# Kernel tuning notes

Hardware: AMD Instinct MI355X
Metric: run time of the kernel (lower is better)

The kernel has to match this reference:

```python
import jax, jax.numpy as jnp
import numpy as np

NEG_SLOPE = 0.2  # PyG GATConv default leaky_relu slope


def segment_softmax(logits, seg, num_segments):
    # logits: [E, H], seg: [E] destination node ids
    m = jax.ops.segment_max(logits, seg, num_segments=num_segments)
    m = jnp.where(jnp.isfinite(m), m, 0.0)  # empty segments
    e = jnp.exp(logits - m[seg])
    s = jax.ops.segment_sum(e, seg, num_segments=num_segments)
    return e / (s[seg] + 1e-16)


def gat_conv(x, src, dst, W, att_src, att_dst, bias, heads, out_ch, concat, num_nodes):
    # x: [N, F_in], W: [F_in, heads*out_ch], att_*: [heads, out_ch]
    h = (x @ W).reshape(num_nodes, heads, out_ch)            # [N, H, C]
    a_src = jnp.sum(h * att_src, axis=-1)                    # [N, H]
    a_dst = jnp.sum(h * att_dst, axis=-1)                    # [N, H]
    logits = jax.nn.leaky_relu(a_src[src] + a_dst[dst], NEG_SLOPE)  # [E, H]
    alpha = segment_softmax(logits, dst, num_nodes)          # [E, H]
    msg = h[src] * alpha[..., None]                          # [E, H, C]
    out = jax.ops.segment_sum(msg, dst, num_segments=num_nodes)  # [N, H, C]
    out = out.reshape(num_nodes, heads * out_ch) if concat else out.mean(axis=1)
    return out + bias


def setup_inputs() -> dict:
    key = jax.random.key(0)
    ks = jax.random.split(key, 12)
    N, E = 50000, 800000
    F_in, Hd, H, F_out = 256, 128, 2, 64

    def glorot(k, shape):
        fan = shape[0] + shape[-1]
        return jax.random.normal(k, shape, dtype=jnp.float32) * jnp.sqrt(2.0 / fan)

    x = jax.random.normal(ks[0], (N, F_in), dtype=jnp.float32)
    edge_index = jax.random.randint(ks[1], (2, E), 0, N, dtype=jnp.int32)
    return {
        "x": x,
        "edge_index": edge_index,
        "W1": glorot(ks[2], (F_in, H * Hd)),
        "att_src1": glorot(ks[3], (H, Hd)),
        "att_dst1": glorot(ks[4], (H, Hd)),
        "b1": jnp.zeros((H * Hd,), dtype=jnp.float32),
        "W2": glorot(ks[5], (H * Hd, F_out)),
        "att_src2": glorot(ks[6], (1, F_out)),
        "att_dst2": glorot(ks[7], (1, F_out)),
        "b2": jnp.zeros((F_out,), dtype=jnp.float32),
    }


def reference(x, edge_index, W1, att_src1, att_dst1, b1, W2, att_src2, att_dst2, b2):
    N = x.shape[0]
    # PyG GATConv default: add self loops
    ar = jnp.arange(N, dtype=edge_index.dtype)
    src = jnp.concatenate([edge_index[0], ar])
    dst = jnp.concatenate([edge_index[1], ar])
    # dropout layers are identity in eval mode
    h = gat_conv(x, src, dst, W1, att_src1, att_dst1, b1,
                 heads=2, out_ch=128, concat=True, num_nodes=N)
    h = jax.nn.elu(h)
    out = gat_conv(h, src, dst, W2, att_src2, att_dst2, b2,
                   heads=1, out_ch=64, concat=False, num_nodes=N)
    return jax.nn.log_softmax(out, axis=1)
```

## Files before the change

kernel.cpp:

```cpp
#include <hip/hip_runtime.h>
#include <hip/hip_bf16.h>

typedef unsigned short u16;
typedef short bf8_t __attribute__((ext_vector_type(8)));
typedef float f32x4 __attribute__((ext_vector_type(4)));

__device__ inline u16 f2bf(float f) {
  unsigned u = __float_as_uint(f);
  u += 0x7FFFu + ((u >> 16) & 1u);
  return (u16)(u >> 16);
}
__device__ inline float bf2f(u16 h) { return __uint_as_float(((unsigned)h) << 16); }
__device__ inline float bflo(unsigned u) { return __uint_as_float(u << 16); }
__device__ inline float bfhi(unsigned u) { return __uint_as_float(u & 0xffff0000u); }

__global__ void prep_kernel(const int* __restrict__ ei, int E, int N, int N8,
                            int* __restrict__ counts,
                            const float* __restrict__ W1, const float* __restrict__ W2,
                            u16* __restrict__ W1T, u16* __restrict__ W2T, int teamBlocks) {
  if ((int)blockIdx.x < teamBlocks) {
    const int team = blockIdx.x & 7;
    const int tslot = blockIdx.x >> 3;
    const int TB = teamBlocks >> 3;
    const int lo = team * N8, hi = min(N, lo + N8);
    const int Et = E + N;
    for (int e = tslot * 256 + (int)threadIdx.x; e < Et; e += TB * 256) {
      int d = (e < E) ? ei[E + e] : (e - E);
      if (d >= lo && d < hi) atomicAdd(&counts[d], 1);
    }
  } else {
    int idx = ((int)blockIdx.x - teamBlocks) * 256 + (int)threadIdx.x;
    if (idx < 256 * 256) {
      int m = idx >> 8, k = idx & 255;
      W1T[idx] = f2bf(W1[k * 256 + m]);
    } else if (idx < 256 * 256 + 64 * 256) {
      int i = idx - 256 * 256;
      int m = i >> 8, k = i & 255;
      W2T[i] = f2bf(W2[k * 64 + m]);
    }
  }
}

__global__ void block_scan_kernel(const int* __restrict__ counts, int* __restrict__ offsets,
                                  int* __restrict__ bsums, int N) {
  __shared__ int sm[256];
  int tid = threadIdx.x;
  int gid = blockIdx.x * 256 + tid;
  int v = (gid < N) ? counts[gid] : 0;
  int val = v;
  sm[tid] = val;
  __syncthreads();
  for (int off = 1; off < 256; off <<= 1) {
    int o = (tid >= off) ? sm[tid - off] : 0;
    __syncthreads();
    val += o;
    sm[tid] = val;
    __syncthreads();
  }
  if (gid < N) offsets[gid] = val - v;
  if (tid == 255) bsums[blockIdx.x] = val;
}

__global__ void scan_sums_kernel(int* __restrict__ bsums, int* __restrict__ offsets,
                                 int nb, int N) {
  __shared__ int sm[1024];
  int tid = threadIdx.x;
  int v = (tid < nb) ? bsums[tid] : 0;
  int val = v;
  sm[tid] = val;
  __syncthreads();
  for (int off = 1; off < 1024; off <<= 1) {
    int o = (tid >= off) ? sm[tid - off] : 0;
    __syncthreads();
    val += o;
    sm[tid] = val;
    __syncthreads();
  }
  if (tid < nb) bsums[tid] = val - v;
  if (tid == 1023) offsets[N] = val;
}

__global__ void add_base_kernel(int* __restrict__ offsets, int* __restrict__ cursor,
                                const int* __restrict__ bsums, int N) {
  int gid = blockIdx.x * 256 + threadIdx.x;
  if (gid >= N) return;
  int o = offsets[gid] + bsums[blockIdx.x];
  offsets[gid] = o;
  cursor[gid] = o;
}

__global__ void scatter_kernel(const int* __restrict__ ei, int E, int N, int N8,
                               int* __restrict__ cursor, int* __restrict__ csr_src,
                               int teamBlocks) {
  const int team = blockIdx.x & 7;
  const int tslot = blockIdx.x >> 3;
  const int TB = teamBlocks >> 3;
  const int lo = team * N8, hi = min(N, lo + N8);
  const int Et = E + N;
  for (int e = tslot * 256 + (int)threadIdx.x; e < Et; e += TB * 256) {
    int d = (e < E) ? ei[E + e] : (e - E);
    if (d >= lo && d < hi) {
      int s = (e < E) ? ei[e] : d;
      int pos = atomicAdd(&cursor[d], 1);
      csr_src[pos] = s;
    }
  }
}

template<int BM, int BN, int BK, int WM, int WN, bool AF32, int EPI>
__global__ __launch_bounds__(256) void mfma_gemm(const void* __restrict__ Ap,
                                                 const u16* __restrict__ Bt,
                                                 u16* __restrict__ C,
                                                 const float* __restrict__ att_s,
                                                 const float* __restrict__ att_d,
                                                 float* __restrict__ a_s,
                                                 float* __restrict__ a_d,
                                                 int N, int K) {
  constexpr int PAD = 8;
  __shared__ u16 As[BM][BK + PAD];
  __shared__ u16 Bs[BN][BK + PAD];
  const int tid = threadIdx.x;
  const int row0 = blockIdx.x * BM;
  const int w = tid >> 6, lane = tid & 63;
  const int wr = (w / (BN / WN)) * WM;
  const int wc = (w % (BN / WN)) * WN;
  constexpr int MF = WM / 16, NF = WN / 16;
  constexpr int CPR = BK / 8;
  f32x4 acc[MF][NF] = {};

  for (int k0 = 0; k0 < K; k0 += BK) {
    constexpr int ACH = BM * CPR;
#pragma unroll
    for (int c = 0; c < ACH; c += 256) {
      int cc = c + tid;
      int r = cc / CPR, kc = cc % CPR;
      int row = row0 + r;
      if (AF32) {
        const float* A = (const float*)Ap;
        float4 v0 = make_float4(0.f, 0.f, 0.f, 0.f), v1 = v0;
        if (row < N) {
          const float* p = A + (size_t)row * K + k0 + kc * 8;
          v0 = *(const float4*)p;
          v1 = *(const float4*)(p + 4);
        }
        union { __hip_bfloat162 h[4]; uint4 u; } cv;
        cv.h[0] = __float22bfloat162_rn(make_float2(v0.x, v0.y));
        cv.h[1] = __float22bfloat162_rn(make_float2(v0.z, v0.w));
        cv.h[2] = __float22bfloat162_rn(make_float2(v1.x, v1.y));
        cv.h[3] = __float22bfloat162_rn(make_float2(v1.z, v1.w));
        *(uint4*)&As[r][kc * 8] = cv.u;
      } else {
        const u16* A = (const u16*)Ap;
        uint4 v = make_uint4(0, 0, 0, 0);
        if (row < N) v = *(const uint4*)(A + (size_t)row * K + k0 + kc * 8);
        *(uint4*)&As[r][kc * 8] = v;
      }
    }
    constexpr int BCH = BN * CPR;
#pragma unroll
    for (int c = 0; c < BCH; c += 256) {
      int cc = c + tid;
      int r = cc / CPR, kc = cc % CPR;
      *(uint4*)&Bs[r][kc * 8] = *(const uint4*)(Bt + (size_t)r * K + k0 + kc * 8);
    }
    __syncthreads();
    const int lr = lane & 15, lk = (lane >> 4) * 8;
    bf8_t a[MF], b[NF];
#pragma unroll
    for (int mi = 0; mi < MF; ++mi) a[mi] = *(bf8_t*)&As[wr + mi * 16 + lr][lk];
#pragma unroll
    for (int ni = 0; ni < NF; ++ni) b[ni] = *(bf8_t*)&Bs[wc + ni * 16 + lr][lk];
#pragma unroll
    for (int mi = 0; mi < MF; ++mi)
#pragma unroll
      for (int ni = 0; ni < NF; ++ni)
        acc[mi][ni] = __builtin_amdgcn_mfma_f32_16x16x32_bf16(a[mi], b[ni], acc[mi][ni], 0, 0, 0);
    __syncthreads();
  }
#pragma unroll
  for (int mi = 0; mi < MF; ++mi)
#pragma unroll
    for (int ni = 0; ni < NF; ++ni)
#pragma unroll
      for (int r = 0; r < 4; ++r) {
        int row = row0 + wr + mi * 16 + (lane >> 4) * 4 + r;
        int col = wc + ni * 16 + (lane & 15);
        if (row < N) C[(size_t)row * BN + col] = f2bf(acc[mi][ni][r]);
      }

  if (EPI == 1) {
    __shared__ float sm_s[4][64];
    __shared__ float sm_d[4][64];
    float asl[NF], adl[NF];
#pragma unroll
    for (int ni = 0; ni < NF; ++ni) {
      asl[ni] = att_s[wc + ni * 16 + (lane & 15)];
      adl[ni] = att_d[wc + ni * 16 + (lane & 15)];
    }
#pragma unroll
    for (int mi = 0; mi < MF; ++mi)
#pragma unroll
      for (int r = 0; r < 4; ++r) {
        float ps = 0.f, pd = 0.f;
#pragma unroll
        for (int ni = 0; ni < NF; ++ni) {
          float c = acc[mi][ni][r];
          ps += c * asl[ni];
          pd += c * adl[ni];
        }
#pragma unroll
        for (int o = 1; o < 16; o <<= 1) {
          ps += __shfl_xor(ps, o);
          pd += __shfl_xor(pd, o);
        }
        if ((lane & 15) == 0) {
          int row = mi * 16 + (lane >> 4) * 4 + r;
          sm_s[w][row] = ps;
          sm_d[w][row] = pd;
        }
      }
    __syncthreads();
    if (tid < 128) {
      int row = tid & 63, head = tid >> 6;
      int grow = row0 + row;
      if (grow < N) {
        a_s[grow * 2 + head] = sm_s[head * 2 + 0][row] + sm_s[head * 2 + 1][row];
        a_d[grow * 2 + head] = sm_d[head * 2 + 0][row] + sm_d[head * 2 + 1][row];
      }
    }
  } else if (EPI == 2) {
    float asl[NF], adl[NF];
#pragma unroll
    for (int ni = 0; ni < NF; ++ni) {
      asl[ni] = att_s[ni * 16 + (lane & 15)];
      adl[ni] = att_d[ni * 16 + (lane & 15)];
    }
#pragma unroll
    for (int mi = 0; mi < MF; ++mi)
#pragma unroll
      for (int r = 0; r < 4; ++r) {
        float ps = 0.f, pd = 0.f;
#pragma unroll
        for (int ni = 0; ni < NF; ++ni) {
          float c = acc[mi][ni][r];
          ps += c * asl[ni];
          pd += c * adl[ni];
        }
#pragma unroll
        for (int o = 1; o < 16; o <<= 1) {
          ps += __shfl_xor(ps, o);
          pd += __shfl_xor(pd, o);
        }
        int row = row0 + wr + mi * 16 + (lane >> 4) * 4 + r;
        if ((lane & 15) == 0 && row < N) {
          a_s[row] = ps;
          a_d[row] = pd;
        }
      }
  }
}

__global__ void agg1_kernel(const u16* __restrict__ H1, const int* __restrict__ offsets,
                            const int* __restrict__ csr_src,
                            const float* __restrict__ a_src, const float* __restrict__ a_dst,
                            const float* __restrict__ b1, u16* __restrict__ out, int N) {
  __shared__ int4 meta[4][64];
  int wv = threadIdx.x >> 6;
  int lane = threadIdx.x & 63;
  int node = blockIdx.x * 4 + wv;
  if (node >= N) return;
  int off = offsets[node];
  int deg = offsets[node + 1] - off;
  float ad0 = a_dst[node * 2 + 0];
  float ad1 = a_dst[node * 2 + 1];
  bool hi = lane >= 32;
  const char* H1c = (const char*)H1;
  const unsigned loff = (unsigned)(lane * 8);
  float4 acc = make_float4(0.f, 0.f, 0.f, 0.f);
  float den = 0.f;
  const int4* mw = meta[wv];

  auto proc = [&](int4 m) {
    float w = hi ? __int_as_float(m.z) : __int_as_float(m.y);
    uint2 u = *(const uint2*)(H1c + (((unsigned)m.x << 9) + loff));
    den += w;
    acc.x += w * bflo(u.x);
    acc.y += w * bfhi(u.x);
    acc.z += w * bflo(u.y);
    acc.w += w * bfhi(u.y);
  };

  for (int base = 0; base < deg; base += 64) {
    int i = base + lane;
    if (i < deg) {
      int s = csr_src[off + i];
      float l0 = a_src[s * 2 + 0] + ad0;
      float l1 = a_src[s * 2 + 1] + ad1;
      l0 = l0 > 0.f ? l0 : 0.2f * l0;
      l1 = l1 > 0.f ? l1 : 0.2f * l1;
      meta[wv][lane] = make_int4(s, __float_as_int(__expf(l0)), __float_as_int(__expf(l1)), 0);
    }
    int cnt = min(64, deg - base);
    int j = 0;
    for (; j + 4 <= cnt; j += 4) {
      int4 m0 = mw[j], m1 = mw[j + 1], m2 = mw[j + 2], m3 = mw[j + 3];
      proc(m0); proc(m1); proc(m2); proc(m3);
    }
    for (; j < cnt; ++j) proc(mw[j]);
  }
  float inv = 1.f / (den + 1e-16f);
  float4 bb = *(const float4*)(b1 + lane * 4);
  float o0 = acc.x * inv + bb.x;
  float o1 = acc.y * inv + bb.y;
  float o2 = acc.z * inv + bb.z;
  float o3 = acc.w * inv + bb.w;
  o0 = o0 > 0.f ? o0 : expm1f(o0);
  o1 = o1 > 0.f ? o1 : expm1f(o1);
  o2 = o2 > 0.f ? o2 : expm1f(o2);
  o3 = o3 > 0.f ? o3 : expm1f(o3);
  uint2 ov;
  ov.x = (unsigned)f2bf(o0) | ((unsigned)f2bf(o1) << 16);
  ov.y = (unsigned)f2bf(o2) | ((unsigned)f2bf(o3) << 16);
  *(uint2*)(out + (size_t)node * 256 + lane * 4) = ov;
}

__global__ void agg2_kernel(const u16* __restrict__ H2, const int* __restrict__ offsets,
                            const int* __restrict__ csr_src,
                            const float* __restrict__ a_src, const float* __restrict__ a_dst,
                            const float* __restrict__ b2, float* __restrict__ out, int N) {
  __shared__ int2 meta[4][64];
  int wv = threadIdx.x >> 6;
  int lane = threadIdx.x & 63;
  int node = blockIdx.x * 4 + wv;
  if (node >= N) return;
  int off = offsets[node];
  int deg = offsets[node + 1] - off;
  float ad = a_dst[node];
  const int grp = lane >> 3;
  const int l3 = lane & 7;
  const char* H2c = (const char*)H2;
  const unsigned loff = (unsigned)(l3 * 16);
  float acc[8] = {0.f, 0.f, 0.f, 0.f, 0.f, 0.f, 0.f, 0.f};
  float den = 0.f;
  const int2* mw = meta[wv];

  auto proc = [&](int jj) {
    int2 m = mw[jj];
    float w = __int_as_float(m.y);
    uint4 u = *(const uint4*)(H2c + (((unsigned)m.x << 7) + loff));
    den += w;
    acc[0] += w * bflo(u.x); acc[1] += w * bfhi(u.x);
    acc[2] += w * bflo(u.y); acc[3] += w * bfhi(u.y);
    acc[4] += w * bflo(u.z); acc[5] += w * bfhi(u.z);
    acc[6] += w * bflo(u.w); acc[7] += w * bfhi(u.w);
  };

  for (int base = 0; base < deg; base += 64) {
    int i = base + lane;
    if (i < deg) {
      int s = csr_src[off + i];
      float l = a_src[s] + ad;
      l = l > 0.f ? l : 0.2f * l;
      meta[wv][lane] = make_int2(s, __float_as_int(__expf(l)));
    }
    int cnt = min(64, deg - base);
    int j = 0;
    for (; j + 16 <= cnt; j += 16) { proc(j + grp); proc(j + 8 + grp); }
    for (; j + 8 <= cnt; j += 8) proc(j + grp);
    int r = cnt - j;
    if (r > 0 && grp < r) proc(j + grp);
  }
#pragma unroll
  for (int k = 0; k < 8; ++k) {
    acc[k] += __shfl_xor(acc[k], 8);
    acc[k] += __shfl_xor(acc[k], 16);
    acc[k] += __shfl_xor(acc[k], 32);
  }
  den += __shfl_xor(den, 8);
  den += __shfl_xor(den, 16);
  den += __shfl_xor(den, 32);

  float inv = 1.f / (den + 1e-16f);
  float4 b01 = *(const float4*)(b2 + l3 * 8);
  float4 b23 = *(const float4*)(b2 + l3 * 8 + 4);
  float bb[8] = {b01.x, b01.y, b01.z, b01.w, b23.x, b23.y, b23.z, b23.w};
  float v[8];
#pragma unroll
  for (int k = 0; k < 8; ++k) v[k] = acc[k] * inv + bb[k];
  float m = v[0];
#pragma unroll
  for (int k = 1; k < 8; ++k) m = fmaxf(m, v[k]);
  m = fmaxf(m, __shfl_xor(m, 1));
  m = fmaxf(m, __shfl_xor(m, 2));
  m = fmaxf(m, __shfl_xor(m, 4));
  float sum = 0.f;
#pragma unroll
  for (int k = 0; k < 8; ++k) sum += __expf(v[k] - m);
  sum += __shfl_xor(sum, 1);
  sum += __shfl_xor(sum, 2);
  sum += __shfl_xor(sum, 4);
  float ls = m + logf(sum);
  if (lane < 8) {
    float4 o0 = make_float4(v[0] - ls, v[1] - ls, v[2] - ls, v[3] - ls);
    float4 o1 = make_float4(v[4] - ls, v[5] - ls, v[6] - ls, v[7] - ls);
    *(float4*)(out + (size_t)node * 64 + l3 * 8) = o0;
    *(float4*)(out + (size_t)node * 64 + l3 * 8 + 4) = o1;
  }
}

extern "C" void kernel_launch(void* const* d_in, const int* in_sizes, int n_in,
                              void* d_out, int out_size, void* d_ws, size_t ws_size,
                              hipStream_t stream) {
  const float* x   = (const float*)d_in[0];
  const int*   ei  = (const int*)d_in[1];
  const float* W1  = (const float*)d_in[2];
  const float* as1 = (const float*)d_in[3];
  const float* ad1 = (const float*)d_in[4];
  const float* b1  = (const float*)d_in[5];
  const float* W2  = (const float*)d_in[6];
  const float* as2 = (const float*)d_in[7];
  const float* ad2 = (const float*)d_in[8];
  const float* b2  = (const float*)d_in[9];
  float* out = (float*)d_out;

  const int N  = in_sizes[0] / 256;
  const int E  = in_sizes[1] / 2;
  const int Et = E + N;
  const int N8 = (N + 7) / 8;
  const int nb  = (N + 255) / 256;
  const int nbt = (256 * 256 + 64 * 256 + 255) / 256;
  const int teamBlocks = 2048;

  char* p = (char*)d_ws;
  auto alloc = [&](size_t bytes) -> char* {
    char* r = p;
    p += (bytes + 255) & ~(size_t)255;
    return r;
  };
  u16* H1b     = (u16*)alloc((size_t)N * 256 * 2);
  u16* h1act   = (u16*)alloc((size_t)N * 256 * 2);
  u16* H2b     = (u16*)alloc((size_t)N * 64 * 2);
  u16* W1T     = (u16*)alloc((size_t)256 * 256 * 2);
  u16* W2T     = (u16*)alloc((size_t)64 * 256 * 2);
  float* a_src1 = (float*)alloc((size_t)N * 2 * 4);
  float* a_dst1 = (float*)alloc((size_t)N * 2 * 4);
  float* a_src2 = (float*)alloc((size_t)N * 4);
  float* a_dst2 = (float*)alloc((size_t)N * 4);
  int* counts   = (int*)alloc((size_t)N * 4);
  int* offsets  = (int*)alloc((size_t)(N + 1) * 4);
  int* cursor   = (int*)alloc((size_t)N * 4);
  int* bsums    = (int*)alloc((size_t)1024 * 4);
  int* csr_src  = (int*)alloc((size_t)Et * 4);

  const int tb = 256;

  hipMemsetAsync(counts, 0, (size_t)N * 4, stream);
  prep_kernel<<<teamBlocks + nbt, tb, 0, stream>>>(ei, E, N, N8, counts, W1, W2, W1T, W2T,
                                                   teamBlocks);
  block_scan_kernel<<<nb, tb, 0, stream>>>(counts, offsets, bsums, N);
  scan_sums_kernel<<<1, 1024, 0, stream>>>(bsums, offsets, nb, N);
  add_base_kernel<<<nb, tb, 0, stream>>>(offsets, cursor, bsums, N);
  scatter_kernel<<<teamBlocks, tb, 0, stream>>>(ei, E, N, N8, cursor, csr_src, teamBlocks);

  mfma_gemm<64, 256, 32, 64, 64, true, 1><<<(N + 63) / 64, tb, 0, stream>>>(
      x, W1T, H1b, as1, ad1, a_src1, a_dst1, N, 256);
  agg1_kernel<<<(N + 3) / 4, tb, 0, stream>>>(H1b, offsets, csr_src, a_src1, a_dst1, b1,
                                              h1act, N);

  mfma_gemm<128, 64, 32, 32, 64, false, 2><<<(N + 127) / 128, tb, 0, stream>>>(
      h1act, W2T, H2b, as2, ad2, a_src2, a_dst2, N, 256);
  agg2_kernel<<<(N + 3) / 4, tb, 0, stream>>>(H2b, offsets, csr_src, a_src2, a_dst2, b2,
                                              out, N);
}
```

Before: 223.6 us.

## Split agg1 across column teams with multi-edge parallel lanes per wave

After: 319.3 us. +42.8%, slower.

```diff
diff --git a/kernel.cpp b/kernel.cpp
--- a/kernel.cpp
+++ b/kernel.cpp
@@ -264,64 +264,63 @@
                             const int* __restrict__ csr_src,
                             const float* __restrict__ a_src, const float* __restrict__ a_dst,
                             const float* __restrict__ b1, u16* __restrict__ out, int N) {
-  __shared__ int4 meta[4][64];
-  int wv = threadIdx.x >> 6;
-  int lane = threadIdx.x & 63;
-  int node = blockIdx.x * 4 + wv;
+  __shared__ int2 meta[4][64];
+  const int team = blockIdx.x & 7;
+  const int wv = threadIdx.x >> 6;
+  const int lane = threadIdx.x & 63;
+  const int node = ((int)blockIdx.x >> 3) * 4 + wv;
   if (node >= N) return;
+  const int head = team >> 2;
+  const int g = lane >> 4;
+  const int l4 = lane & 15;
   int off = offsets[node];
   int deg = offsets[node + 1] - off;
-  float ad0 = a_dst[node * 2 + 0];
-  float ad1 = a_dst[node * 2 + 1];
-  bool hi = lane >= 32;
+  float ad = a_dst[node * 2 + head];
   const char* H1c = (const char*)H1;
-  const unsigned loff = (unsigned)(lane * 8);
-  float4 acc = make_float4(0.f, 0.f, 0.f, 0.f);
-  float den = 0.f;
-  const int4* mw = meta[wv];
-
-  auto proc = [&](int4 m) {
-    float w = hi ? __int_as_float(m.z) : __int_as_float(m.y);
-    uint2 u = *(const uint2*)(H1c + (((unsigned)m.x << 9) + loff));
+  const unsigned coff = (unsigned)(team * 64 + l4 * 4);
+  float a0 = 0.f, a1 = 0.f, den = 0.f;
+  const int2* mw = meta[wv];
+
+  auto proc = [&](int jj) {
+    int2 m = mw[jj];
+    float w = __int_as_float(m.y);
+    unsigned u = *(const unsigned*)(H1c + (((unsigned)m.x << 9) + coff));
     den += w;
-    acc.x += w * bflo(u.x);
-    acc.y += w * bfhi(u.x);
-    acc.z += w * bflo(u.y);
-    acc.w += w * bfhi(u.y);
+    a0 += w * bflo(u);
+    a1 += w * bfhi(u);
   };
 
   for (int base = 0; base < deg; base += 64) {
     int i = base + lane;
     if (i < deg) {
       int s = csr_src[off + i];
-      float l0 = a_src[s * 2 + 0] + ad0;
-      float l1 = a_src[s * 2 + 1] + ad1;
-      l0 = l0 > 0.f ? l0 : 0.2f * l0;
-      l1 = l1 > 0.f ? l1 : 0.2f * l1;
-      meta[wv][lane] = make_int4(s, __float_as_int(__expf(l0)), __float_as_int(__expf(l1)), 0);
+      float l = a_src[s * 2 + head] + ad;
+      l = l > 0.f ? l : 0.2f * l;
+      meta[wv][lane] = make_int2(s, __float_as_int(__expf(l)));
     }
     int cnt = min(64, deg - base);
     int j = 0;
-    for (; j + 4 <= cnt; j += 4) {
-      int4 m0 = mw[j], m1 = mw[j + 1], m2 = mw[j + 2], m3 = mw[j + 3];
-      proc(m0); proc(m1); proc(m2); proc(m3);
-    }
-    for (; j < cnt; ++j) proc(mw[j]);
-  }
+    for (; j + 16 <= cnt; j += 16) {
+      proc(j + g); proc(j + 4 + g); proc(j + 8 + g); proc(j + 12 + g);
+    }
+    for (; j + 4 <= cnt; j += 4) proc(j + g);
+    int r = cnt - j;
+    if (g < r) proc(j + g);
+  }
+  a0 += __shfl_xor(a0, 16); a0 += __shfl_xor(a0, 32);
+  a1 += __shfl_xor(a1, 16); a1 += __shfl_xor(a1, 32);
+  den += __shfl_xor(den, 16); den += __shfl_xor(den, 32);
+
   float inv = 1.f / (den + 1e-16f);
-  float4 bb = *(const float4*)(b1 + lane * 4);
-  float o0 = acc.x * inv + bb.x;
-  float o1 = acc.y * inv + bb.y;
-  float o2 = acc.z * inv + bb.z;
-  float o3 = acc.w * inv + bb.w;
+  float2 bb = *(const float2*)(b1 + team * 32 + l4 * 2);
+  float o0 = a0 * inv + bb.x;
+  float o1 = a1 * inv + bb.y;
   o0 = o0 > 0.f ? o0 : expm1f(o0);
   o1 = o1 > 0.f ? o1 : expm1f(o1);
-  o2 = o2 > 0.f ? o2 : expm1f(o2);
-  o3 = o3 > 0.f ? o3 : expm1f(o3);
-  uint2 ov;
-  ov.x = (unsigned)f2bf(o0) | ((unsigned)f2bf(o1) << 16);
-  ov.y = (unsigned)f2bf(o2) | ((unsigned)f2bf(o3) << 16);
-  *(uint2*)(out + (size_t)node * 256 + lane * 4) = ov;
+  if (g == 0) {
+    unsigned ov = (unsigned)f2bf(o0) | ((unsigned)f2bf(o1) << 16);
+    *(unsigned*)((char*)out + (((size_t)node) << 9) + coff) = ov;
+  }
 }
 
 __global__ void agg2_kernel(const u16* __restrict__ H2, const int* __restrict__ offsets,
@@ -464,8 +463,8 @@
 
   mfma_gemm<64, 256, 32, 64, 64, true, 1><<<(N + 63) / 64, tb, 0, stream>>>(
       x, W1T, H1b, as1, ad1, a_src1, a_dst1, N, 256);
-  agg1_kernel<<<(N + 3) / 4, tb, 0, stream>>>(H1b, offsets, csr_src, a_src1, a_dst1, b1,
-                                              h1act, N);
+  agg1_kernel<<<((N + 3) / 4) * 8, tb, 0, stream>>>(H1b, offsets, csr_src, a_src1, a_dst1,
+                                                    b1, h1act, N);
 
   mfma_gemm<128, 64, 32, 32, 64, false, 2><<<(N + 127) / 128, tb, 0, stream>>>(
       h1act, W2T, H2b, as2, ad2, a_src2, a_dst2, N, 256);
```
